# Performance work log

Measured on AMD Instinct MI355X. Metric: run time of the kernel, lower is better.

## Reference

```python
import jax, jax.numpy as jnp
import numpy as np

B, T, C = 4, 4096, 128

def setup_inputs() -> dict:
    key = jax.random.key(0)
    k1, k2, k3, k4 = jax.random.split(key, 4)
    x = jax.random.normal(k1, (B, T, C), dtype=jnp.float32)
    s = 1.0 / np.sqrt(C)
    Wq = jax.random.normal(k2, (C, C), dtype=jnp.float32) * s
    Wk = jax.random.normal(k3, (C, C), dtype=jnp.float32) * s
    Wv = jax.random.normal(k4, (C, C), dtype=jnp.float32) * s
    return {"x": x, "Wq": Wq, "Wk": Wk, "Wv": Wv}

def reference(x, Wq, Wk, Wv):
    # nn.Linear(bias=False): y = x @ W.T
    q = jnp.einsum('btc,dc->btd', x, Wq)
    k = jnp.einsum('btc,dc->btd', x, Wk)
    v = jnp.einsum('btc,dc->btd', x, Wv)
    scale = 1.0 / jnp.sqrt(jnp.asarray(x.shape[-1], x.dtype))
    att = jnp.einsum('btd,bsd->bts', q, k) * scale  # [B,T,T]
    causal = jnp.tril(jnp.ones((x.shape[1], x.shape[1]), dtype=bool))
    att = jnp.where(causal[None, :, :], att, -jnp.inf)
    w = jax.nn.softmax(att, axis=-1)
    # dropout p=0.0 -> identity
    out = jnp.einsum('bts,bsd->btd', w, v)
    return out
```

## Files before the change

### kernel.cpp

```cpp
#include <hip/hip_runtime.h>
#include <hip/hip_bf16.h>
#include <math.h>

#define T_SEQ 4096
#define C_DIM 128
#define B_SZ  4

typedef __attribute__((ext_vector_type(8))) short short8;
typedef __attribute__((ext_vector_type(4))) short short4v;
typedef __attribute__((ext_vector_type(4))) float f32x4;

__device__ __forceinline__ short f2bf(float f) {
    union { float fv; unsigned u; } v; v.fv = f;
    unsigned r = v.u + 0x7fff + ((v.u >> 16) & 1);
    return (short)(r >> 16);
}

__device__ __forceinline__ unsigned pk_bf16(float a, float b) {
    union { __hip_bfloat162 h2; unsigned u; } c;
    c.h2 = __float22bfloat162_rn(make_float2(a, b));
    return c.u;
}

__device__ __forceinline__ short8 load_f32x8_bf16(const float* p) {
    const float4* q = (const float4*)p;
    float4 a = q[0], b = q[1];
    short8 r;
    r[0] = f2bf(a.x); r[1] = f2bf(a.y); r[2] = f2bf(a.z); r[3] = f2bf(a.w);
    r[4] = f2bf(b.x); r[5] = f2bf(b.y); r[6] = f2bf(b.z); r[7] = f2bf(b.w);
    return r;
}

__device__ __forceinline__ void async_cp16(const short* g, short* l) {
    __builtin_amdgcn_global_load_lds(
        (const __attribute__((address_space(1))) unsigned int*)g,
        (__attribute__((address_space(3))) unsigned int*)l, 16, 0, 0);
}

__global__ __launch_bounds__(512) void qkv_proj(
    const float* __restrict__ x, const float* __restrict__ Wq,
    const float* __restrict__ Wk, const float* __restrict__ Wv,
    short* __restrict__ Q, short* __restrict__ Kf, short* __restrict__ Vf)
{
    __shared__ short8 Wl[2048];

    const int tid  = threadIdx.x;
    const int lane = tid & 63;
    const int ln15 = lane & 15;
    const int quad = lane >> 4;
    const int mat  = blockIdx.x >> 6;
    const int rt   = (blockIdx.x & 63) * 8 + (tid >> 6);
    const int m0   = rt * 32;

    const float* W = (mat == 0) ? Wq : (mat == 1) ? Wk : Wv;

    for (int i = tid; i < 2048; i += 512) {
        int n = i >> 4, kc = i & 15;
        short8 v = load_f32x8_bf16(W + n * C_DIM + kc * 8);
        Wl[((n >> 4) * 4 + (kc >> 2)) * 64 + (kc & 3) * 16 + (n & 15)] = v;
    }

    short8 afr[2][4];
#pragma unroll
    for (int ms = 0; ms < 2; ++ms) {
        const float* xrow = x + (size_t)(m0 + ms * 16 + ln15) * C_DIM + quad * 8;
#pragma unroll
        for (int ks = 0; ks < 4; ++ks)
            afr[ms][ks] = load_f32x8_bf16(xrow + ks * 32);
    }

    __syncthreads();

    const float scale = (mat == 0) ? (0.08838834764831845f * 1.4426950408889634f)
                                   : 1.0f;
    const int b  = m0 >> 12;
    const int tl = m0 & 4095;

#pragma unroll
    for (int nt = 0; nt < 8; ++nt) {
        f32x4 acc0 = {0.f, 0.f, 0.f, 0.f};
        f32x4 acc1 = {0.f, 0.f, 0.f, 0.f};
#pragma unroll
        for (int ks = 0; ks < 4; ++ks) {
            short8 bfr = Wl[(nt * 4 + ks) * 64 + lane];
            if (mat == 2) {
                acc0 = __builtin_amdgcn_mfma_f32_16x16x32_bf16(afr[0][ks], bfr, acc0, 0, 0, 0);
                acc1 = __builtin_amdgcn_mfma_f32_16x16x32_bf16(afr[1][ks], bfr, acc1, 0, 0, 0);
            } else {
                acc0 = __builtin_amdgcn_mfma_f32_16x16x32_bf16(bfr, afr[0][ks], acc0, 0, 0, 0);
                acc1 = __builtin_amdgcn_mfma_f32_16x16x32_bf16(bfr, afr[1][ks], acc1, 0, 0, 0);
            }
        }
        if (mat == 0) {
            short4v s0, s1;
#pragma unroll
            for (int r = 0; r < 4; ++r) { s0[r] = f2bf(acc0[r] * scale); s1[r] = f2bf(acc1[r] * scale); }
            *(short4v*)&Q[(size_t)(m0 + ln15) * C_DIM + nt * 16 + quad * 4]      = s0;
            *(short4v*)&Q[(size_t)(m0 + 16 + ln15) * C_DIM + nt * 16 + quad * 4] = s1;
        } else if (mat == 1) {
            const int t16 = tl >> 4;
            short4v s0, s1;
#pragma unroll
            for (int r = 0; r < 4; ++r) { s0[r] = f2bf(acc0[r]); s1[r] = f2bf(acc1[r]); }
            size_t base = (((size_t)(b * 256 + t16) * 4 + (nt >> 1)) << 9)
                        + (((nt & 1) * 2 + (quad >> 1)) * 128) + ln15 * 8 + (quad & 1) * 4;
            *(short4v*)&Kf[base]        = s0;
            *(short4v*)&Kf[base + 2048] = s1;
        } else {
            const int kvc = tl >> 5;
            short4v s0, s1;
#pragma unroll
            for (int r = 0; r < 4; ++r) { s0[r] = f2bf(acc0[r]); s1[r] = f2bf(acc1[r]); }
            short* vbase = Vf + (((size_t)(b * 128 + kvc) * 8 + nt) << 9);
            *(short4v*)&vbase[((quad >> 1) * 16 + ln15) * 8 + (quad & 1) * 4]       = s0;
            *(short4v*)&vbase[(((quad >> 1) + 2) * 16 + ln15) * 8 + (quad & 1) * 4] = s1;
        }
    }
}

__global__ __launch_bounds__(256, 1) void flash_attn(
    const short* __restrict__ Q, const short* __restrict__ Kf,
    const short* __restrict__ Vf, float* __restrict__ part,
    float* __restrict__ lpart)
{
    __shared__ short Klds[2][16384];
    __shared__ short Vlds[2][16384];
    __shared__ short Plds[64 * 132];
    __shared__ float lsum[64];

    const int tid  = threadIdx.x;
    const int w    = tid >> 6;
    const int lane = tid & 63;
    const int ln15 = lane & 15;
    const int quad = lane >> 4;
    const int bid  = blockIdx.x;
    const int x    = bid & 7;
    const int b    = x >> 1;
    const int h    = x & 1;
    const int j    = bid >> 3;

    const short* Qb = Q  + (size_t)b * T_SEQ * C_DIM;
    const short* Kb = Kf + ((size_t)b << 19);
    const short* Vb = Vf + ((size_t)b << 19);

    for (int half = 0; half < 2; ++half) {
        const int qc   = half ? (63 - j) : j;
        const int q0   = qc * 64;
        const int kmax = (qc * 64 + 63) >> 7;

        short8 qf[4][4];
#pragma unroll
        for (int qt = 0; qt < 4; ++qt) {
            const short* qrow = Qb + (size_t)(q0 + qt * 16 + ln15) * C_DIM + quad * 8;
#pragma unroll
            for (int ks = 0; ks < 4; ++ks)
                qf[qt][ks] = *(const short8*)(qrow + ks * 32);
        }

        f32x4 acc[4][2];
#pragma unroll
        for (int qt = 0; qt < 4; ++qt)
#pragma unroll
            for (int d = 0; d < 2; ++d)
                acc[qt][d] = (f32x4){0.f, 0.f, 0.f, 0.f};
        float l_i[4] = {0.f, 0.f, 0.f, 0.f};

        if (h <= kmax) {
            const short* gk = Kb + ((size_t)h << 14) + w * 4096;
            const short* gv = Vb + ((size_t)h << 14) + w * 4096;
#pragma unroll
            for (int i = 0; i < 8; ++i) {
                async_cp16(gk + i * 512 + lane * 8, &Klds[0][w * 4096 + i * 512]);
                async_cp16(gv + i * 512 + lane * 8, &Vlds[0][w * 4096 + i * 512]);
            }
        }

        int idx = 0;
        for (int r = h; r <= kmax; r += 2, ++idx) {
            const int cur = idx & 1;
            const int kv0 = r << 7;

            __syncthreads();

            if (r + 2 <= kmax) {
                const short* gk = Kb + ((size_t)(r + 2) << 14) + w * 4096;
                const short* gv = Vb + ((size_t)(r + 2) << 14) + w * 4096;
                short* lk = &Klds[cur ^ 1][w * 4096];
                short* lv = &Vlds[cur ^ 1][w * 4096];
#pragma unroll
                for (int i = 0; i < 8; ++i) {
                    async_cp16(gk + i * 512 + lane * 8, lk + i * 512);
                    async_cp16(gv + i * 512 + lane * 8, lv + i * 512);
                }
            }

            short8 kfr[2][4];
#pragma unroll
            for (int i = 0; i < 2; ++i)
#pragma unroll
                for (int ks = 0; ks < 4; ++ks)
                    kfr[i][ks] = *(const short8*)&Klds[cur][((w * 2 + i) * 4 + ks) * 512 + lane * 8];

            f32x4 St[2][4];
#pragma unroll
            for (int i = 0; i < 2; ++i)
#pragma unroll
                for (int qt = 0; qt < 4; ++qt) {
                    f32x4 s = {0.f, 0.f, 0.f, 0.f};
#pragma unroll
                    for (int ks = 0; ks < 4; ++ks)
                        s = __builtin_amdgcn_mfma_f32_16x16x32_bf16(kfr[i][ks], qf[qt][ks], s, 0, 0, 0);
                    St[i][qt] = s;
                }

            if (kv0 + 128 > q0) {
#pragma unroll
                for (int i = 0; i < 2; ++i)
#pragma unroll
                    for (int qt = 0; qt < 4; ++qt) {
                        int qcol = q0 + qt * 16 + ln15;
#pragma unroll
                        for (int rr = 0; rr < 4; ++rr)
                            if (kv0 + (w * 2 + i) * 16 + quad * 4 + rr > qcol)
                                St[i][qt][rr] = -INFINITY;
                    }
            }

#pragma unroll
            for (int i = 0; i < 2; ++i)
#pragma unroll
                for (int qt = 0; qt < 4; ++qt) {
                    float p0 = __builtin_amdgcn_exp2f(St[i][qt][0] - 16.f);
                    float p1 = __builtin_amdgcn_exp2f(St[i][qt][1] - 16.f);
                    float p2 = __builtin_amdgcn_exp2f(St[i][qt][2] - 16.f);
                    float p3 = __builtin_amdgcn_exp2f(St[i][qt][3] - 16.f);
                    l_i[qt] += (p0 + p1) + (p2 + p3);
                    uint2 pk;
                    pk.x = pk_bf16(p0, p1);
                    pk.y = pk_bf16(p2, p3);
                    *(uint2*)&Plds[(qt * 16 + ln15) * 132 + (w * 2 + i) * 16 + quad * 4] = pk;
                }

            __syncthreads();

#pragma unroll
            for (int kc = 0; kc < 4; ++kc) {
                short8 vfr[2];
#pragma unroll
                for (int d = 0; d < 2; ++d)
                    vfr[d] = *(const short8*)&Vlds[cur][(kc * 8 + w * 2 + d) * 512 + lane * 8];
#pragma unroll
                for (int qt = 0; qt < 4; ++qt) {
                    short8 pf = *(const short8*)&Plds[(qt * 16 + ln15) * 132 + kc * 32 + quad * 8];
#pragma unroll
                    for (int d = 0; d < 2; ++d)
                        acc[qt][d] = __builtin_amdgcn_mfma_f32_16x16x32_bf16(vfr[d], pf, acc[qt][d], 0, 0, 0);
                }
            }
        }

        __syncthreads();
        if (tid < 64) lsum[tid] = 0.f;
        __syncthreads();
#pragma unroll
        for (int qt = 0; qt < 4; ++qt)
            atomicAdd(&lsum[qt * 16 + ln15], l_i[qt]);
        __syncthreads();

        const size_t pb = ((size_t)((h * 4 + b) * 64 + qc)) * 8192;
#pragma unroll
        for (int qt = 0; qt < 4; ++qt)
#pragma unroll
            for (int d = 0; d < 2; ++d) {
                float4 v = make_float4(acc[qt][d][0], acc[qt][d][1],
                                       acc[qt][d][2], acc[qt][d][3]);
                *(float4*)&part[pb + (qt * 16 + ln15) * 128 + (w * 2 + d) * 16 + quad * 4] = v;
            }
        if (tid < 64)
            lpart[(size_t)((h * 4 + b) * 64 + qc) * 64 + tid] = lsum[tid];
        __syncthreads();
    }
}

__global__ __launch_bounds__(256) void combine(
    const float* __restrict__ part, const float* __restrict__ lpart,
    float* __restrict__ out)
{
    const int tid = threadIdx.x;
    const int bid = blockIdx.x;
    const size_t PLANE  = (size_t)4 * 64 * 8192;
    const size_t LPLANE = (size_t)4 * 64 * 64;

#pragma unroll
    for (int i = 0; i < 8; ++i) {
        int f4  = bid * 2048 + i * 256 + tid;
        int c4  = f4 & 31;
        int row = f4 >> 5;
        int b   = row >> 12;
        int t   = row & 4095;
        int qc  = t >> 6;
        int qr  = t & 63;
        size_t base = (size_t)((b * 64 + qc)) * 8192 + qr * 128 + c4 * 4;
        float4 p0 = *(const float4*)&part[base];
        float4 p1 = *(const float4*)&part[base + PLANE];
        float  l  = lpart[(size_t)(b * 64 + qc) * 64 + qr]
                  + lpart[(size_t)(b * 64 + qc) * 64 + qr + LPLANE];
        float li = 1.0f / l;
        float4 v;
        v.x = (p0.x + p1.x) * li;
        v.y = (p0.y + p1.y) * li;
        v.z = (p0.z + p1.z) * li;
        v.w = (p0.w + p1.w) * li;
        ((float4*)out)[f4] = v;
    }
}

extern "C" void kernel_launch(void* const* d_in, const int* in_sizes, int n_in,
                              void* d_out, int out_size, void* d_ws, size_t ws_size,
                              hipStream_t stream) {
    const float* x  = (const float*)d_in[0];
    const float* Wq = (const float*)d_in[1];
    const float* Wk = (const float*)d_in[2];
    const float* Wv = (const float*)d_in[3];
    float* out = (float*)d_out;

    const size_t elems = (size_t)B_SZ * T_SEQ * C_DIM;
    short* Q  = (short*)d_ws;
    short* Kf = Q  + elems;
    short* Vf = Kf + elems;
    float* part  = (float*)(Vf + elems);
    float* lpart = part + (size_t)2 * 4 * 64 * 8192;

    hipLaunchKernelGGL(qkv_proj, dim3(192), dim3(512), 0, stream,
                       x, Wq, Wk, Wv, Q, Kf, Vf);
    hipLaunchKernelGGL(flash_attn, dim3(256), dim3(256), 0, stream,
                       Q, Kf, Vf, part, lpart);
    hipLaunchKernelGGL(combine, dim3(256), dim3(256), 0, stream,
                       part, lpart, out);
}
```

Before: 127.9 us.

## Split flash attention block across eight waves instead of four

Doubles the flash_attn workgroup from 256 to 512 threads. Each wave now computes scores for one 16-row K tile instead of two. The PV stage is split into a 2x4 grid over query tiles and head-dimension tiles, which halves the per-wave accumulator and score registers. The intent is more waves to hide MFMA, LDS and exp latency within the one block per CU that the large LDS footprint allows. The cost is more per-wave overhead: every wave still holds the full Q fragment and reloads P fragments, and barriers now span more waves.

```diff
diff --git a/kernel.cpp b/kernel.cpp
--- a/kernel.cpp
+++ b/kernel.cpp
@@ -118,7 +118,7 @@
     }
 }
 
-__global__ __launch_bounds__(256, 1) void flash_attn(
+__global__ __launch_bounds__(512, 2) void flash_attn(
     const short* __restrict__ Q, const short* __restrict__ Kf,
     const short* __restrict__ Vf, float* __restrict__ part,
     float* __restrict__ lpart)
@@ -133,6 +133,8 @@
     const int lane = tid & 63;
     const int ln15 = lane & 15;
     const int quad = lane >> 4;
+    const int qg   = w >> 2;
+    const int dg   = w & 3;
     const int bid  = blockIdx.x;
     const int x    = bid & 7;
     const int b    = x >> 1;
@@ -157,21 +159,21 @@
                 qf[qt][ks] = *(const short8*)(qrow + ks * 32);
         }
 
-        f32x4 acc[4][2];
-#pragma unroll
-        for (int qt = 0; qt < 4; ++qt)
-#pragma unroll
-            for (int d = 0; d < 2; ++d)
-                acc[qt][d] = (f32x4){0.f, 0.f, 0.f, 0.f};
+        f32x4 acc[2][2];
+#pragma unroll
+        for (int qi = 0; qi < 2; ++qi)
+#pragma unroll
+            for (int di = 0; di < 2; ++di)
+                acc[qi][di] = (f32x4){0.f, 0.f, 0.f, 0.f};
         float l_i[4] = {0.f, 0.f, 0.f, 0.f};
 
         if (h <= kmax) {
-            const short* gk = Kb + ((size_t)h << 14) + w * 4096;
-            const short* gv = Vb + ((size_t)h << 14) + w * 4096;
-#pragma unroll
-            for (int i = 0; i < 8; ++i) {
-                async_cp16(gk + i * 512 + lane * 8, &Klds[0][w * 4096 + i * 512]);
-                async_cp16(gv + i * 512 + lane * 8, &Vlds[0][w * 4096 + i * 512]);
+            const short* gk = Kb + ((size_t)h << 14) + w * 2048;
+            const short* gv = Vb + ((size_t)h << 14) + w * 2048;
+#pragma unroll
+            for (int i = 0; i < 4; ++i) {
+                async_cp16(gk + i * 512 + lane * 8, &Klds[0][w * 2048 + i * 512]);
+                async_cp16(gv + i * 512 + lane * 8, &Vlds[0][w * 2048 + i * 512]);
             }
         }
 
@@ -183,63 +185,55 @@
             __syncthreads();
 
             if (r + 2 <= kmax) {
-                const short* gk = Kb + ((size_t)(r + 2) << 14) + w * 4096;
-                const short* gv = Vb + ((size_t)(r + 2) << 14) + w * 4096;
-                short* lk = &Klds[cur ^ 1][w * 4096];
-                short* lv = &Vlds[cur ^ 1][w * 4096];
-#pragma unroll
-                for (int i = 0; i < 8; ++i) {
+                const short* gk = Kb + ((size_t)(r + 2) << 14) + w * 2048;
+                const short* gv = Vb + ((size_t)(r + 2) << 14) + w * 2048;
+                short* lk = &Klds[cur ^ 1][w * 2048];
+                short* lv = &Vlds[cur ^ 1][w * 2048];
+#pragma unroll
+                for (int i = 0; i < 4; ++i) {
                     async_cp16(gk + i * 512 + lane * 8, lk + i * 512);
                     async_cp16(gv + i * 512 + lane * 8, lv + i * 512);
                 }
             }
 
-            short8 kfr[2][4];
-#pragma unroll
-            for (int i = 0; i < 2; ++i)
+            short8 kfr[4];
+#pragma unroll
+            for (int ks = 0; ks < 4; ++ks)
+                kfr[ks] = *(const short8*)&Klds[cur][(w * 4 + ks) * 512 + lane * 8];
+
+            f32x4 St[4];
+#pragma unroll
+            for (int qt = 0; qt < 4; ++qt) {
+                f32x4 s = {0.f, 0.f, 0.f, 0.f};
 #pragma unroll
                 for (int ks = 0; ks < 4; ++ks)
-                    kfr[i][ks] = *(const short8*)&Klds[cur][((w * 2 + i) * 4 + ks) * 512 + lane * 8];
-
-            f32x4 St[2][4];
-#pragma unroll
-            for (int i = 0; i < 2; ++i)
+                    s = __builtin_amdgcn_mfma_f32_16x16x32_bf16(kfr[ks], qf[qt][ks], s, 0, 0, 0);
+                St[qt] = s;
+            }
+
+            if (kv0 + 128 > q0) {
 #pragma unroll
                 for (int qt = 0; qt < 4; ++qt) {
-                    f32x4 s = {0.f, 0.f, 0.f, 0.f};
-#pragma unroll
-                    for (int ks = 0; ks < 4; ++ks)
-                        s = __builtin_amdgcn_mfma_f32_16x16x32_bf16(kfr[i][ks], qf[qt][ks], s, 0, 0, 0);
-                    St[i][qt] = s;
+                    int qcol = q0 + qt * 16 + ln15;
+#pragma unroll
+                    for (int rr = 0; rr < 4; ++rr)
+                        if (kv0 + w * 16 + quad * 4 + rr > qcol)
+                            St[qt][rr] = -INFINITY;
                 }
-
-            if (kv0 + 128 > q0) {
-#pragma unroll
-                for (int i = 0; i < 2; ++i)
-#pragma unroll
-                    for (int qt = 0; qt < 4; ++qt) {
-                        int qcol = q0 + qt * 16 + ln15;
-#pragma unroll
-                        for (int rr = 0; rr < 4; ++rr)
-                            if (kv0 + (w * 2 + i) * 16 + quad * 4 + rr > qcol)
-                                St[i][qt][rr] = -INFINITY;
-                    }
-            }
-
-#pragma unroll
-            for (int i = 0; i < 2; ++i)
-#pragma unroll
-                for (int qt = 0; qt < 4; ++qt) {
-                    float p0 = __builtin_amdgcn_exp2f(St[i][qt][0] - 16.f);
-                    float p1 = __builtin_amdgcn_exp2f(St[i][qt][1] - 16.f);
-                    float p2 = __builtin_amdgcn_exp2f(St[i][qt][2] - 16.f);
-                    float p3 = __builtin_amdgcn_exp2f(St[i][qt][3] - 16.f);
-                    l_i[qt] += (p0 + p1) + (p2 + p3);
-                    uint2 pk;
-                    pk.x = pk_bf16(p0, p1);
-                    pk.y = pk_bf16(p2, p3);
-                    *(uint2*)&Plds[(qt * 16 + ln15) * 132 + (w * 2 + i) * 16 + quad * 4] = pk;
-                }
+            }
+
+#pragma unroll
+            for (int qt = 0; qt < 4; ++qt) {
+                float p0 = __builtin_amdgcn_exp2f(St[qt][0] - 16.f);
+                float p1 = __builtin_amdgcn_exp2f(St[qt][1] - 16.f);
+                float p2 = __builtin_amdgcn_exp2f(St[qt][2] - 16.f);
+                float p3 = __builtin_amdgcn_exp2f(St[qt][3] - 16.f);
+                l_i[qt] += (p0 + p1) + (p2 + p3);
+                uint2 pk;
+                pk.x = pk_bf16(p0, p1);
+                pk.y = pk_bf16(p2, p3);
+                *(uint2*)&Plds[(qt * 16 + ln15) * 132 + w * 16 + quad * 4] = pk;
+            }
 
             __syncthreads();
 
@@ -247,14 +241,14 @@
             for (int kc = 0; kc < 4; ++kc) {
                 short8 vfr[2];
 #pragma unroll
-                for (int d = 0; d < 2; ++d)
-                    vfr[d] = *(const short8*)&Vlds[cur][(kc * 8 + w * 2 + d) * 512 + lane * 8];
-#pragma unroll
-                for (int qt = 0; qt < 4; ++qt) {
-                    short8 pf = *(const short8*)&Plds[(qt * 16 + ln15) * 132 + kc * 32 + quad * 8];
-#pragma unroll
-                    for (int d = 0; d < 2; ++d)
-                        acc[qt][d] = __builtin_amdgcn_mfma_f32_16x16x32_bf16(vfr[d], pf, acc[qt][d], 0, 0, 0);
+                for (int di = 0; di < 2; ++di)
+                    vfr[di] = *(const short8*)&Vlds[cur][(kc * 8 + dg * 2 + di) * 512 + lane * 8];
+#pragma unroll
+                for (int qi = 0; qi < 2; ++qi) {
+                    short8 pf = *(const short8*)&Plds[((qg * 2 + qi) * 16 + ln15) * 132 + kc * 32 + quad * 8];
+#pragma unroll
+                    for (int di = 0; di < 2; ++di)
+                        acc[qi][di] = __builtin_amdgcn_mfma_f32_16x16x32_bf16(vfr[di], pf, acc[qi][di], 0, 0, 0);
                 }
             }
         }
@@ -269,12 +263,13 @@
 
         const size_t pb = ((size_t)((h * 4 + b) * 64 + qc)) * 8192;
 #pragma unroll
-        for (int qt = 0; qt < 4; ++qt)
-#pragma unroll
-            for (int d = 0; d < 2; ++d) {
-                float4 v = make_float4(acc[qt][d][0], acc[qt][d][1],
-                                       acc[qt][d][2], acc[qt][d][3]);
-                *(float4*)&part[pb + (qt * 16 + ln15) * 128 + (w * 2 + d) * 16 + quad * 4] = v;
+        for (int qi = 0; qi < 2; ++qi)
+#pragma unroll
+            for (int di = 0; di < 2; ++di) {
+                float4 v = make_float4(acc[qi][di][0], acc[qi][di][1],
+                                       acc[qi][di][2], acc[qi][di][3]);
+                *(float4*)&part[pb + ((qg * 2 + qi) * 16 + ln15) * 128
+                                + (dg * 2 + di) * 16 + quad * 4] = v;
             }
         if (tid < 64)
             lpart[(size_t)((h * 4 + b) * 64 + qc) * 64 + tid] = lsum[tid];
@@ -333,7 +328,7 @@
 
     hipLaunchKernelGGL(qkv_proj, dim3(192), dim3(512), 0, stream,
                        x, Wq, Wk, Wv, Q, Kf, Vf);
-    hipLaunchKernelGGL(flash_attn, dim3(256), dim3(256), 0, stream,
+    hipLaunchKernelGGL(flash_attn, dim3(256), dim3(512), 0, stream,
                        Q, Kf, Vf, part, lpart);
     hipLaunchKernelGGL(combine, dim3(256), dim3(256), 0, stream,
                        part, lpart, out);
```

New measurement: 125.8 us. Within noise of the previous version (-1.6%).
